# Kernel optimization log

Measured on AMD Instinct MI355X. Metric: run time of the kernel, lower is better.

## Reference

```python
import jax, jax.numpy as jnp
import numpy as np

R = 21
STRIDE = 2
ETA = 0.01
H = W = 147
HP = WP = 64
PI = np.pi
TAU = 0.1


def _unfold(img):
    # img: (N, C, H, W) -> patches (N, C, R, R, HP, WP), patch[h,w] starts at (h*STRIDE, w*STRIDE)
    hidx = jnp.arange(HP) * STRIDE          # (HP,)
    widx = jnp.arange(WP) * STRIDE          # (WP,)
    ridx = jnp.arange(R)
    rows = hidx[:, None] + ridx[None, :]    # (HP, R)
    cols = widx[:, None] + ridx[None, :]    # (WP, R)
    p = img[:, :, rows, :]                  # (N, C, HP, R, W)
    p = p[:, :, :, :, cols]                 # (N, C, HP, R, WP, R)
    return jnp.transpose(p, (0, 1, 3, 5, 2, 4))  # (N, C, R, R, HP, WP)


def _params2dists(params, x, y, tau=TAU):
    # params: (N, 5, HP, WP); x, y: (1, R, R, 1, 1)
    x0 = params[:, 3][:, None, None]        # (N,1,1,HP,WP)
    y0 = params[:, 4][:, None, None]
    ang = jnp.sort(jnp.mod(params[:, :3], 2 * PI), axis=1)
    a1 = ang[:, 0][:, None, None]
    a2 = ang[:, 1][:, None, None]
    a3 = ang[:, 2][:, None, None]
    a4 = 0.5 * (a1 + a3) + jnp.where(jnp.mod(0.5 * (a1 - a3), 2 * PI) >= PI, PI, 0.0)

    def g(dtheta):
        return (dtheta / PI - 1.0) ** 35

    def line(a):
        # signed distance to line through (x0,y0) at angle a: (N, R, R, HP, WP)
        return -jnp.sin(a) * (x - x0) + jnp.cos(a) * (y - y0)

    sgn42 = jnp.where(jnp.mod(a2 - a4, 2 * PI) < PI, 1.0, -1.0)
    dist42 = sgn42 * jnp.minimum(sgn42 * line(a4), -sgn42 * line(a2)) + g(jnp.mod(a2 - a4, 2 * PI)) * tau
    sgn13 = jnp.where(jnp.mod(a3 - a1, 2 * PI) < PI, 1.0, -1.0)
    dist13 = sgn13 * jnp.minimum(sgn13 * line(a1), -sgn13 * line(a3)) + g(jnp.mod(a3 - a1, 2 * PI)) * tau
    return jnp.stack([dist13, dist42], axis=1)  # (N, 2, R, R, HP, WP)


def _dists2indicators(dists):
    h = 0.5 * (1.0 + (2.0 / PI) * jnp.arctan(dists / ETA))
    return jnp.stack([1.0 - h[:, 0],
                      h[:, 0] * (1.0 - h[:, 1]),
                      h[:, 0] * h[:, 1]], axis=1)  # (N, 3, R, R, HP, WP)


def setup_inputs() -> dict:
    key = jax.random.key(0)
    k1, k2, k3 = jax.random.split(key, 3)
    ests = jax.random.normal(k1, (1, HP * WP, 5), dtype=jnp.float32)
    noisy_image = jax.random.uniform(k2, (1, H, W, 3), dtype=jnp.float32)
    gt_image = jax.random.uniform(k3, (1, H, W, 3), dtype=jnp.float32)
    return {"ests": ests, "noisy_image": noisy_image, "gt_image": gt_image, "alpha": 1}


def reference(ests, noisy_image, gt_image, alpha):
    # colors_only=True path of Assistance.forward
    grid = jnp.linspace(-1.0, 1.0, R)
    yv, xv = jnp.meshgrid(grid, grid, indexing="ij")
    x = xv.reshape(1, R, R, 1, 1)
    y = yv.reshape(1, R, R, 1, 1)

    e = jnp.transpose(ests, (0, 2, 1)).reshape(1, 5, HP, WP)
    angles = jnp.sort(jnp.mod((e[:, :3] + 1.0) * PI, 2 * PI), axis=1)
    x0y0 = e[:, 3:] * 3.0
    para = jnp.concatenate([angles, x0y0], axis=1)   # (1, 5, HP, WP)

    img_patches = _unfold(jnp.transpose(noisy_image, (0, 3, 1, 2)))  # (1,3,R,R,HP,WP)

    dists = _params2dists(para, x, y)
    wedges = _dists2indicators(dists)                # (1,3,R,R,HP,WP)
    # numerator: sum over patch pixels of img * wedge indicator
    num = jnp.einsum("ncrshw,nkrshw->nckhw", img_patches, wedges)
    wsum = wedges.sum(axis=(2, 3))                   # (1,3,HP,WP)
    colors = num / (wsum[:, None] + 1e-10)           # (1,3,3,HP,WP)
    return colors
```

## Files before the change

### kernel.cpp

```cpp
#include <hip/hip_runtime.h>
#include <hip/hip_bf16.h>
#include <math.h>

#define HPX 64
#define WPX 64
#define IMGW 147
#define PI_F 3.14159265358979323846f
#define TWO_PI_F 6.28318530717958647692f
#define INV_TWO_PI_F 0.15915494309189533577f
#define INV_PI_F 0.31830988618379067154f
#define TAU_F 0.1f

__device__ __forceinline__ float mod2pi(float x) {
    float t = floorf(x * INV_TWO_PI_F);
    return fmaf(-t, TWO_PI_F, x);
}

__device__ __forceinline__ float gpow35(float dtheta) {
    float t = dtheta * INV_PI_F - 1.f;
    float t2 = t * t;
    float t4 = t2 * t2;
    float t8 = t4 * t4;
    float t16 = t8 * t8;
    float t32 = t16 * t16;
    return t32 * t2 * t;
}

__device__ __forceinline__ float fast_h(float d) {
    float z = d * 100.f;
    float az = fabsf(z);
    bool big = az > 1.0f;
    float r = big ? __builtin_amdgcn_rcpf(az) : az;
    float a = r * r;
    float pol = r * fmaf(a, fmaf(a, fmaf(a, -0.0851330f, 0.1801410f), -0.3302995f),
                         0.9998660f);
    float res = big ? (1.5707963267948966f - pol) : pol;
    res = copysignf(res, z);
    return fmaf(res, INV_PI_F, 0.5f);
}

__global__ __launch_bounds__(256) void wedge_colors_kernel(
    const float* __restrict__ ests,
    const float* __restrict__ img,
    float* __restrict__ out)
{
    const int wave = threadIdx.x >> 6;
    const int lane = threadIdx.x & 63;
    const int p = blockIdx.x * 4 + wave;
    const int ph = p >> 6;
    const int pw = p & 63;

    const float* e = ests + p * 5;
    float b0 = mod2pi((e[0] + 1.f) * PI_F);
    float b1 = mod2pi((e[1] + 1.f) * PI_F);
    float b2 = mod2pi((e[2] + 1.f) * PI_F);
    float a1 = fminf(b0, fminf(b1, b2));
    float a3 = fmaxf(b0, fmaxf(b1, b2));
    float a2 = fmaxf(fminf(b0, b1), fminf(fmaxf(b0, b1), b2));
    float x0 = e[3] * 3.f;
    float y0 = e[4] * 3.f;

    float mhalf = mod2pi(0.5f * (a1 - a3));
    float a4 = 0.5f * (a1 + a3) + (mhalf >= PI_F ? PI_F : 0.f);

    float d42m = mod2pi(a2 - a4);
    float d13m = mod2pi(a3 - a1);
    float sgn42 = (d42m < PI_F) ? 1.f : -1.f;
    float sgn13 = (d13m < PI_F) ? 1.f : -1.f;
    float g42 = gpow35(d42m) * TAU_F;
    float g13 = gpow35(d13m) * TAU_F;

    float s1 = __sinf(a1), c1 = __cosf(a1);
    float s2 = __sinf(a2), c2 = __cosf(a2);
    float s3 = __sinf(a3), c3 = __cosf(a3);
    float s4 = __sinf(a4), c4 = __cosf(a4);

    const int r_off = lane / 21;
    const int s     = lane - 21 * r_off;
    float x  = (float)s * 0.1f - 1.f;
    float dx = x - x0;

    float P1 =  sgn13 * c1, B1 = -sgn13 * s1 * dx;
    float P3 = -sgn13 * c3, B3 =  sgn13 * s3 * dx;
    float P4 =  sgn42 * c4, B4 = -sgn42 * s4 * dx;
    float P2 = -sgn42 * c2, B2 =  sgn42 * s2 * dx;

    float sp0 = 0.f, sp1 = 0.f, sp2 = 0.f;
    float sa0 = 0.f, sa1 = 0.f, sa2 = 0.f;
    float sb0 = 0.f, sb1 = 0.f, sb2 = 0.f;
    float sh = 0.f, su = 0.f;

    if (lane < 63) {
        const float* base = img + ((2 * ph + r_off) * IMGW + (2 * pw + s)) * 3;
#pragma unroll
        for (int k = 0; k < 7; k++) {
            int r = r_off + 3 * k;
            float y  = (float)r * 0.1f - 1.f;
            float dy = y - y0;

            const float* px = base + k * (3 * IMGW * 3);
            float p0 = px[0];
            float p1 = px[1];
            float p2 = px[2];

            float t1 = fmaf(P1, dy, B1);
            float t3 = fmaf(P3, dy, B3);
            float t4 = fmaf(P4, dy, B4);
            float t2 = fmaf(P2, dy, B2);

            float d13 = fmaf(sgn13, fminf(t1, t3), g13);
            float d42 = fmaf(sgn42, fminf(t4, t2), g42);

            float h0 = fast_h(d13);
            float h1 = fast_h(d42);
            float u  = h0 * h1;

            sp0 += p0;            sp1 += p1;            sp2 += p2;
            sa0 = fmaf(p0, h0, sa0); sa1 = fmaf(p1, h0, sa1); sa2 = fmaf(p2, h0, sa2);
            sb0 = fmaf(p0, u, sb0);  sb1 = fmaf(p1, u, sb1);  sb2 = fmaf(p2, u, sb2);
            sh += h0;             su += u;
        }
    }

#pragma unroll
    for (int off = 32; off > 0; off >>= 1) {
        sp0 += __shfl_xor(sp0, off, 64); sp1 += __shfl_xor(sp1, off, 64); sp2 += __shfl_xor(sp2, off, 64);
        sa0 += __shfl_xor(sa0, off, 64); sa1 += __shfl_xor(sa1, off, 64); sa2 += __shfl_xor(sa2, off, 64);
        sb0 += __shfl_xor(sb0, off, 64); sb1 += __shfl_xor(sb1, off, 64); sb2 += __shfl_xor(sb2, off, 64);
        sh  += __shfl_xor(sh,  off, 64); su  += __shfl_xor(su,  off, 64);
    }

    if (lane == 0) {
        float inv0 = 1.f / (441.f - sh + 1e-10f);
        float inv1 = 1.f / (sh - su + 1e-10f);
        float inv2 = 1.f / (su + 1e-10f);
        const int base = ph * WPX + pw;
        out[0 * 4096 + base] = (sp0 - sa0) * inv0;
        out[1 * 4096 + base] = (sa0 - sb0) * inv1;
        out[2 * 4096 + base] = sb0 * inv2;
        out[3 * 4096 + base] = (sp1 - sa1) * inv0;
        out[4 * 4096 + base] = (sa1 - sb1) * inv1;
        out[5 * 4096 + base] = sb1 * inv2;
        out[6 * 4096 + base] = (sp2 - sa2) * inv0;
        out[7 * 4096 + base] = (sa2 - sb2) * inv1;
        out[8 * 4096 + base] = sb2 * inv2;
    }
}

extern "C" void kernel_launch(void* const* d_in, const int* in_sizes, int n_in,
                              void* d_out, int out_size, void* d_ws, size_t ws_size,
                              hipStream_t stream) {
    const float* ests  = (const float*)d_in[0];
    const float* noisy = (const float*)d_in[1];
    float* out = (float*)d_out;

    wedge_colors_kernel<<<1024, 256, 0, stream>>>(ests, noisy, out);
}
```

Measured before the change: 66.09 us.

## Split patch rows across two waves, reduce via LDS and DPP wave sums

Each patch is now processed by two waves, which split its 7 row-steps 4/3, doubling the grid to 2048 blocks. The second wave's partial sums are combined through shared memory, and the cross-lane reduction uses DPP row-shift and broadcast adds instead of shuffle-xor, with the result read from lane 63. The ×100 scale is folded into the line coefficients and the g terms, and launch bounds now request 6 blocks per CU. The aim is more parallelism and lower per-wave latency for this small grid, at the cost of a __syncthreads, LDS traffic, an idle half-wave during the final reduction, and per-patch setup done twice.

After: 65.93 us. No clear change (-0.2%).

```diff
diff --git a/kernel.cpp b/kernel.cpp
--- a/kernel.cpp
+++ b/kernel.cpp
@@ -1,9 +1,6 @@
 #include <hip/hip_runtime.h>
-#include <hip/hip_bf16.h>
 #include <math.h>
 
-#define HPX 64
-#define WPX 64
 #define IMGW 147
 #define PI_F 3.14159265358979323846f
 #define TWO_PI_F 6.28318530717958647692f
@@ -26,8 +23,7 @@
     return t32 * t2 * t;
 }
 
-__device__ __forceinline__ float fast_h(float d) {
-    float z = d * 100.f;
+__device__ __forceinline__ float fast_h_z(float z) {
     float az = fabsf(z);
     bool big = az > 1.0f;
     float r = big ? __builtin_amdgcn_rcpf(az) : az;
@@ -39,16 +35,35 @@
     return fmaf(res, INV_PI_F, 0.5f);
 }
 
-__global__ __launch_bounds__(256) void wedge_colors_kernel(
+template <int CTRL>
+__device__ __forceinline__ float dpp_add(float x) {
+    int y = __builtin_amdgcn_update_dpp(0, __float_as_int(x), CTRL, 0xf, 0xf, true);
+    return x + __int_as_float(y);
+}
+__device__ __forceinline__ float wave_sum63(float x) {
+    x = dpp_add<0x111>(x);
+    x = dpp_add<0x112>(x);
+    x = dpp_add<0x114>(x);
+    x = dpp_add<0x118>(x);
+    x = dpp_add<0x142>(x);
+    x = dpp_add<0x143>(x);
+    return x;
+}
+
+__global__ __launch_bounds__(256, 6) void wedge_colors_kernel(
     const float* __restrict__ ests,
     const float* __restrict__ img,
     float* __restrict__ out)
 {
     const int wave = threadIdx.x >> 6;
     const int lane = threadIdx.x & 63;
-    const int p = blockIdx.x * 4 + wave;
-    const int ph = p >> 6;
-    const int pw = p & 63;
+    const int half = wave & 1;
+    const int pp   = wave >> 1;
+    const int p    = blockIdx.x * 2 + pp;
+    const int ph   = p >> 6;
+    const int pw   = p & 63;
+
+    __shared__ float red[2][64][11];
 
     const float* e = ests + p * 5;
     float b0 = mod2pi((e[0] + 1.f) * PI_F);
@@ -67,8 +82,8 @@
     float d13m = mod2pi(a3 - a1);
     float sgn42 = (d42m < PI_F) ? 1.f : -1.f;
     float sgn13 = (d13m < PI_F) ? 1.f : -1.f;
-    float g42 = gpow35(d42m) * TAU_F;
-    float g13 = gpow35(d13m) * TAU_F;
+    float g13z = gpow35(d13m) * (TAU_F * 100.f);
+    float g42z = gpow35(d42m) * (TAU_F * 100.f);
 
     float s1 = __sinf(a1), c1 = __cosf(a1);
     float s2 = __sinf(a2), c2 = __cosf(a2);
@@ -80,70 +95,75 @@
     float x  = (float)s * 0.1f - 1.f;
     float dx = x - x0;
 
-    float P1 =  sgn13 * c1, B1 = -sgn13 * s1 * dx;
-    float P3 = -sgn13 * c3, B3 =  sgn13 * s3 * dx;
-    float P4 =  sgn42 * c4, B4 = -sgn42 * s4 * dx;
-    float P2 = -sgn42 * c2, B2 =  sgn42 * s2 * dx;
+    float P1 = (sgn13 * c1) * 100.f, B1 = (-sgn13 * s1 * dx) * 100.f;
+    float P3 = (-sgn13 * c3) * 100.f, B3 = (sgn13 * s3 * dx) * 100.f;
+    float P4 = (sgn42 * c4) * 100.f, B4 = (-sgn42 * s4 * dx) * 100.f;
+    float P2 = (-sgn42 * c2) * 100.f, B2 = (sgn42 * s2 * dx) * 100.f;
 
-    float sp0 = 0.f, sp1 = 0.f, sp2 = 0.f;
-    float sa0 = 0.f, sa1 = 0.f, sa2 = 0.f;
-    float sb0 = 0.f, sb1 = 0.f, sb2 = 0.f;
-    float sh = 0.f, su = 0.f;
+    float acc[11];
+#pragma unroll
+    for (int q = 0; q < 11; q++) acc[q] = 0.f;
 
     if (lane < 63) {
         const float* base = img + ((2 * ph + r_off) * IMGW + (2 * pw + s)) * 3;
-#pragma unroll
-        for (int k = 0; k < 7; k++) {
-            int r = r_off + 3 * k;
-            float y  = (float)r * 0.1f - 1.f;
-            float dy = y - y0;
 
-            const float* px = base + k * (3 * IMGW * 3);
-            float p0 = px[0];
-            float p1 = px[1];
-            float p2 = px[2];
+#define BODY(K) {                                                         \
+        const float* px = base + (K) * (3 * IMGW * 3);                    \
+        float p0 = px[0], p1 = px[1], p2 = px[2];                         \
+        float yy = (float)(r_off + 3 * (K)) * 0.1f - 1.f;                 \
+        float dy = yy - y0;                                               \
+        float t1 = fmaf(P1, dy, B1);                                      \
+        float t3 = fmaf(P3, dy, B3);                                      \
+        float t4 = fmaf(P4, dy, B4);                                      \
+        float t2 = fmaf(P2, dy, B2);                                      \
+        float z13 = fmaf(sgn13, fminf(t1, t3), g13z);                     \
+        float z42 = fmaf(sgn42, fminf(t4, t2), g42z);                     \
+        float h0 = fast_h_z(z13);                                         \
+        float h1 = fast_h_z(z42);                                         \
+        float u  = h0 * h1;                                               \
+        acc[0] += p0; acc[1] += p1; acc[2] += p2;                         \
+        acc[3] = fmaf(p0, h0, acc[3]);                                    \
+        acc[4] = fmaf(p1, h0, acc[4]);                                    \
+        acc[5] = fmaf(p2, h0, acc[5]);                                    \
+        acc[6] = fmaf(p0, u, acc[6]);                                     \
+        acc[7] = fmaf(p1, u, acc[7]);                                     \
+        acc[8] = fmaf(p2, u, acc[8]);                                     \
+        acc[9] += h0; acc[10] += u; }
 
-            float t1 = fmaf(P1, dy, B1);
-            float t3 = fmaf(P3, dy, B3);
-            float t4 = fmaf(P4, dy, B4);
-            float t2 = fmaf(P2, dy, B2);
-
-            float d13 = fmaf(sgn13, fminf(t1, t3), g13);
-            float d42 = fmaf(sgn42, fminf(t4, t2), g42);
-
-            float h0 = fast_h(d13);
-            float h1 = fast_h(d42);
-            float u  = h0 * h1;
-
-            sp0 += p0;            sp1 += p1;            sp2 += p2;
-            sa0 = fmaf(p0, h0, sa0); sa1 = fmaf(p1, h0, sa1); sa2 = fmaf(p2, h0, sa2);
-            sb0 = fmaf(p0, u, sb0);  sb1 = fmaf(p1, u, sb1);  sb2 = fmaf(p2, u, sb2);
-            sh += h0;             su += u;
-        }
+        if (half == 0) { BODY(0) BODY(1) BODY(2) BODY(3) }
+        else           { BODY(4) BODY(5) BODY(6) }
+#undef BODY
     }
 
+    if (half) {
 #pragma unroll
-    for (int off = 32; off > 0; off >>= 1) {
-        sp0 += __shfl_xor(sp0, off, 64); sp1 += __shfl_xor(sp1, off, 64); sp2 += __shfl_xor(sp2, off, 64);
-        sa0 += __shfl_xor(sa0, off, 64); sa1 += __shfl_xor(sa1, off, 64); sa2 += __shfl_xor(sa2, off, 64);
-        sb0 += __shfl_xor(sb0, off, 64); sb1 += __shfl_xor(sb1, off, 64); sb2 += __shfl_xor(sb2, off, 64);
-        sh  += __shfl_xor(sh,  off, 64); su  += __shfl_xor(su,  off, 64);
+        for (int q = 0; q < 11; q++) red[pp][lane][q] = acc[q];
     }
+    __syncthreads();
 
-    if (lane == 0) {
-        float inv0 = 1.f / (441.f - sh + 1e-10f);
-        float inv1 = 1.f / (sh - su + 1e-10f);
-        float inv2 = 1.f / (su + 1e-10f);
-        const int base = ph * WPX + pw;
-        out[0 * 4096 + base] = (sp0 - sa0) * inv0;
-        out[1 * 4096 + base] = (sa0 - sb0) * inv1;
-        out[2 * 4096 + base] = sb0 * inv2;
-        out[3 * 4096 + base] = (sp1 - sa1) * inv0;
-        out[4 * 4096 + base] = (sa1 - sb1) * inv1;
-        out[5 * 4096 + base] = sb1 * inv2;
-        out[6 * 4096 + base] = (sp2 - sa2) * inv0;
-        out[7 * 4096 + base] = (sa2 - sb2) * inv1;
-        out[8 * 4096 + base] = sb2 * inv2;
+    if (!half) {
+#pragma unroll
+        for (int q = 0; q < 11; q++) acc[q] += red[pp][lane][q];
+
+#pragma unroll
+        for (int q = 0; q < 11; q++) acc[q] = wave_sum63(acc[q]);
+
+        if (lane == 63) {
+            float sh = acc[9], su = acc[10];
+            float inv0 = 1.f / (441.f - sh + 1e-10f);
+            float inv1 = 1.f / (sh - su + 1e-10f);
+            float inv2 = 1.f / (su + 1e-10f);
+            const int base = ph * 64 + pw;
+            out[0 * 4096 + base] = (acc[0] - acc[3]) * inv0;
+            out[1 * 4096 + base] = (acc[3] - acc[6]) * inv1;
+            out[2 * 4096 + base] = acc[6] * inv2;
+            out[3 * 4096 + base] = (acc[1] - acc[4]) * inv0;
+            out[4 * 4096 + base] = (acc[4] - acc[7]) * inv1;
+            out[5 * 4096 + base] = acc[7] * inv2;
+            out[6 * 4096 + base] = (acc[2] - acc[5]) * inv0;
+            out[7 * 4096 + base] = (acc[5] - acc[8]) * inv1;
+            out[8 * 4096 + base] = acc[8] * inv2;
+        }
     }
 }
 
@@ -154,5 +174,5 @@
     const float* noisy = (const float*)d_in[1];
     float* out = (float*)d_out;
 
-    wedge_colors_kernel<<<1024, 256, 0, stream>>>(ests, noisy, out);
+    wedge_colors_kernel<<<2048, 256, 0, stream>>>(ests, noisy, out);
 }
```
